# Performance work log

Hardware: AMD Instinct MI355X
Metric: run time of the kernel (lower is better)

The kernel has to match this reference:

```python
import jax, jax.numpy as jnp
import numpy as np

# dims
P = 49      # per-participant input dim
G = 8       # group-only (dyadic/triadic) dim
R = 26      # robot input dim
PH = 20     # participant GRU hidden dim
GF = 16     # group_fc output dim
H = 64      # main RNN hidden dim
T = 512     # seq_len
B = 2048    # batch
D = 2 * P + G + R  # 132 total feature dim, layout [p1|p2|group|robot]


def _gru_cell(x, h, Wih, Whh, bih, bhh):
    # torch.nn.GRUCell math: gates ordered (r, z, n)
    gi = x @ Wih.T + bih          # (B, 3*hid)
    gh = h @ Whh.T + bhh          # (B, 3*hid)
    ir, iz, inn = jnp.split(gi, 3, axis=-1)
    hr, hz, hn = jnp.split(gh, 3, axis=-1)
    r = jax.nn.sigmoid(ir + hr)
    z = jax.nn.sigmoid(iz + hz)
    n = jnp.tanh(inn + r * hn)
    return (1.0 - z) * n + z * h


def setup_inputs() -> dict:
    key = jax.random.key(0)
    ks = jax.random.split(key, 16)

    def u(k, shape, fan):
        b = 1.0 / np.sqrt(fan)
        return jax.random.uniform(k, shape, jnp.float32, -b, b)

    rnn_in = GF + R  # 42: group_fc output concat robot slice
    return {
        "sequence": jax.random.normal(ks[0], (T, B, D), jnp.float32),
        # p1 GRUCell
        "p1_Wih": u(ks[1], (3 * PH, P), PH),
        "p1_Whh": u(ks[2], (3 * PH, PH), PH),
        "p1_bih": u(ks[3], (3 * PH,), PH),
        "p1_bhh": u(ks[4], (3 * PH,), PH),
        # p2 GRUCell
        "p2_Wih": u(ks[5], (3 * PH, P), PH),
        "p2_Whh": u(ks[6], (3 * PH, PH), PH),
        "p2_bih": u(ks[7], (3 * PH,), PH),
        "p2_bhh": u(ks[8], (3 * PH,), PH),
        # group_fc: Linear(2*PH+G -> GF) + ReLU
        "g_W": u(ks[9], (GF, 2 * PH + G), 2 * PH + G),
        "g_b": u(ks[10], (GF,), 2 * PH + G),
        # main GRUCell
        "r_Wih": u(ks[11], (3 * H, rnn_in), H),
        "r_Whh": u(ks[12], (3 * H, H), H),
        "r_bih": u(ks[13], (3 * H,), H),
        "r_bhh": u(ks[14], (3 * H,), H),
    }


def reference(sequence, p1_Wih, p1_Whh, p1_bih, p1_bhh,
              p2_Wih, p2_Whh, p2_bih, p2_bhh,
              g_W, g_b, r_Wih, r_Whh, r_bih, r_bhh):
    batch = sequence.shape[1]

    def step(carry, xt):
        h1, h2, h = carry
        # data_helper slices: [p1 | p2 | group | robot]
        x_p1 = xt[:, :P]
        x_p2 = xt[:, P:2 * P]
        x_g = xt[:, 2 * P:2 * P + G]
        x_r = xt[:, 2 * P + G:]
        h1 = _gru_cell(x_p1, h1, p1_Wih, p1_Whh, p1_bih, p1_bhh)
        h2 = _gru_cell(x_p2, h2, p2_Wih, p2_Whh, p2_bih, p2_bhh)
        g = jax.nn.relu(jnp.concatenate([h1, h2, x_g], axis=1) @ g_W.T + g_b)
        inp = jnp.concatenate([g, x_r], axis=1)  # (B, GF+R)
        h = _gru_cell(inp, h, r_Wih, r_Whh, r_bih, r_bhh)
        return (h1, h2, h), h

    init = (jnp.zeros((batch, PH), jnp.float32),
            jnp.zeros((batch, PH), jnp.float32),
            jnp.zeros((batch, H), jnp.float32))
    _, all_hidden = jax.lax.scan(step, init, sequence)  # (T, B, H)
    return all_hidden
```

## Files before the change

### kernel.cpp

```cpp
#include <hip/hip_runtime.h>


#define T_STEPS 512
#define B_BATCH 2048
#define D_IN    132
#define NROWS   8
#define NBLOCKS 256
#define STEP2   (B_BATCH * D_IN / 2)
#define NITEMS  (NROWS * 66)

typedef _Float16 f16x8 __attribute__((ext_vector_type(8)));
typedef float    f32x4 __attribute__((ext_vector_type(4)));
typedef float    f32x2 __attribute__((ext_vector_type(2)));

#define MFMA16(a, b, c) __builtin_amdgcn_mfma_f32_16x16x32_f16((a), (b), (c), 0, 0, 0)

#define PX    1024
#define AP1   0
#define AP2   2048
#define AG    4096
#define AR    8192
#define AP1H  12288
#define AP2H  14336
#define AH    16384
#define LDS_N 18432

#define BARRIER() do { \
    asm volatile("s_waitcnt lgkmcnt(0)\n\ts_barrier" ::: "memory"); \
    __builtin_amdgcn_sched_barrier(0); \
  } while (0)

__device__ __forceinline__ int swz(int row, int col) {
  return row * 64 + (((col >> 3) ^ (row & 7)) << 3) + (col & 7);
}

__device__ __forceinline__ f16x8 ldsFrag(const _Float16* lds, int base, int lane, int kt) {
  int row = lane & 7;
  int blk = ((kt << 2) + (lane >> 4)) ^ row;
  return *reinterpret_cast<const f16x8*>(lds + base + row * 64 + blk * 8);
}

__device__ __forceinline__ f16x8 mkfrag(const float* W, int row, int K, int kbase, int lane, bool ok) {
  f16x8 f;
  int k0 = kbase + ((lane >> 4) << 3);
#pragma unroll
  for (int j = 0; j < 8; ++j) {
    int k = k0 + j;
    float v = 0.0f;
    if (ok && k < K) v = W[row * K + k];
    f[j] = (_Float16)v;
  }
  return f;
}

__device__ __forceinline__ float rcpf(float x) { return __builtin_amdgcn_rcpf(x); }
__device__ __forceinline__ float ex2(float x)  { return __builtin_amdgcn_exp2f(x); }

__global__ __launch_bounds__(512, 2) void rnn_fused(
    const float* __restrict__ seq,
    const float* __restrict__ p1Wih, const float* __restrict__ p1Whh,
    const float* __restrict__ p1bih, const float* __restrict__ p1bhh,
    const float* __restrict__ p2Wih, const float* __restrict__ p2Whh,
    const float* __restrict__ p2bih, const float* __restrict__ p2bhh,
    const float* __restrict__ gW,    const float* __restrict__ gb,
    const float* __restrict__ rWih,  const float* __restrict__ rWhh,
    const float* __restrict__ rbih,  const float* __restrict__ rbhh,
    float* __restrict__ out)
{
  __shared__ __align__(16) _Float16 lds[LDS_N];
  const int tid  = threadIdx.x;
  const int lane = tid & 63;
  const int wv   = tid >> 6;
  const bool isR = (wv < 4);
  const int b0   = blockIdx.x * NROWS;
  const int ul   = lane & 15;
  const bool lo  = (lane < 32);
  const int grp4 = ((lane >> 4) & 1) * 4;
  const int row0 = grp4 + (lo ? 0 : 2);
  const float C1 = 1.44269504089f;

  for (int i = tid; i < LDS_N; i += 512) lds[i] = (_Float16)0.0f;

  f16x8 fghr[2], fghz[2], fghn[2], fgir[2], fgiz[2], fgin[2];
  float nbr2 = 0, nbz2 = 0, bin2 = 0, bhn2 = 0;
  float hq2[2] = {0, 0};
  int stAddr[3][2]; int ldIdx[3] = {0, 0, 0};
  bool stOK[3] = {false, false, false}, isP[3] = {false, false, false};
  int ahw2[2] = {0, 0};
  float* outp = nullptr;

  f16x8 pgi0[2], pgi1[2], pgi2[2], pgh0, pgh1, pgh2, fgw[2];
  float nbr = 0, nbz = 0, bin = 0, bhn = 0, gbias = 0;
  float h1q2[2] = {0, 0};
  int apB = 0, aphB = 0, up = 0; bool uok = false;
  int agw2[2] = {0, 0}, aphw2[2] = {0, 0}, arw2[2] = {0, 0};

  if (isR) {
    const int uR = wv * 16 + ul;
    fghr[0] = mkfrag(rWhh,       uR, 64,  0, lane, true);
    fghr[1] = mkfrag(rWhh,       uR, 64, 32, lane, true);
    fghz[0] = mkfrag(rWhh,  64 + uR, 64,  0, lane, true);
    fghz[1] = mkfrag(rWhh,  64 + uR, 64, 32, lane, true);
    fghn[0] = mkfrag(rWhh, 128 + uR, 64,  0, lane, true);
    fghn[1] = mkfrag(rWhh, 128 + uR, 64, 32, lane, true);
    fgir[0] = mkfrag(rWih,       uR, 42,  0, lane, true);
    fgir[1] = mkfrag(rWih,       uR, 42, 32, lane, true);
    fgiz[0] = mkfrag(rWih,  64 + uR, 42,  0, lane, true);
    fgiz[1] = mkfrag(rWih,  64 + uR, 42, 32, lane, true);
    fgin[0] = mkfrag(rWih, 128 + uR, 42,  0, lane, true);
    fgin[1] = mkfrag(rWih, 128 + uR, 42, 32, lane, true);
    nbr2 = -C1 * (rbih[uR] + rbhh[uR]);
    nbz2 = -C1 * (rbih[64 + uR] + rbhh[64 + uR]);
    bin2 = rbih[128 + uR]; bhn2 = rbhh[128 + uR];
    ahw2[0] = AH + swz(row0, uR);
    ahw2[1] = AH + swz(row0 + 1, uR);
#pragma unroll
    for (int it = 0; it < 3; ++it) {
      int ii = it * 256 + (wv * 64 + lane);
      stOK[it] = (ii < NITEMS);
      int iic = stOK[it] ? ii : (NITEMS - 1);
      ldIdx[it] = iic;
      int rr = iic / 66, c2 = iic % 66;
      isP[it] = (c2 < 49);
#pragma unroll
      for (int e = 0; e < 2; ++e) {
        int c = c2 * 2 + e;
        int tb, col;
        if (c < 49)       { tb = AP1; col = c; }
        else if (c < 98)  { tb = AP2; col = c - 49; }
        else if (c < 106) { tb = AG;  col = 40 + (c - 98); }
        else              { tb = AR;  col = 16 + (c - 106); }
        stAddr[it][e] = tb + swz(rr, col);
      }
    }
    outp = out + (size_t)(b0 + row0) * 64 + uR;
  } else {
    const int pw  = wv - 4;
    const int gru = pw >> 1;
    const int s   = pw & 1;
    const float* Wih = gru ? p2Wih : p1Wih;
    const float* Whh = gru ? p2Whh : p1Whh;
    const float* bih = gru ? p2bih : p1bih;
    const float* bhh = gru ? p2bhh : p1bhh;
    up  = s * 16 + ul;
    uok = (up < 20);
    pgi0[0] = mkfrag(Wih,      up, 49,  0, lane, uok);
    pgi0[1] = mkfrag(Wih,      up, 49, 32, lane, uok);
    pgh0    = mkfrag(Whh,      up, 20,  0, lane, uok);
    pgi1[0] = mkfrag(Wih, 20 + up, 49,  0, lane, uok);
    pgi1[1] = mkfrag(Wih, 20 + up, 49, 32, lane, uok);
    pgh1    = mkfrag(Whh, 20 + up, 20,  0, lane, uok);
    pgi2[0] = mkfrag(Wih, 40 + up, 49,  0, lane, uok);
    pgi2[1] = mkfrag(Wih, 40 + up, 49, 32, lane, uok);
    pgh2    = mkfrag(Whh, 40 + up, 20,  0, lane, uok);
    fgw[0]  = mkfrag(gW, ul, 48,  0, lane, true);
    fgw[1]  = mkfrag(gW, ul, 48, 32, lane, true);
    gbias = gb[ul];
    if (uok) {
      nbr = -C1 * (bih[up] + bhh[up]);
      nbz = -C1 * (bih[20 + up] + bhh[20 + up]);
      bin = bih[40 + up]; bhn = bhh[40 + up];
    }
    apB  = gru ? AP2  : AP1;
    aphB = gru ? AP2H : AP1H;
    const int gcol = gru ? (20 + up) : up;
#pragma unroll
    for (int j = 0; j < 2; ++j) {
      agw2[j]  = AG + swz(row0 + j, gcol);
      aphw2[j] = aphB + swz(row0 + j, up);
      arw2[j]  = AR + swz(row0 + j, ul);
    }
  }

  __syncthreads();

  f32x2 rs0[3], rs1[3], rs2[3], rs3[3];
  const f32x2* spR = nullptr;
  if (isR) {
    const f32x2* sp = reinterpret_cast<const f32x2*>(seq) + (size_t)b0 * (D_IN / 2);
#pragma unroll
    for (int it = 0; it < 3; ++it) {
      rs0[it] = sp[ldIdx[it]];
      rs1[it] = sp[(size_t)1 * STEP2 + ldIdx[it]];
      rs2[it] = sp[(size_t)2 * STEP2 + ldIdx[it]];
      rs3[it] = sp[(size_t)3 * STEP2 + ldIdx[it]];
    }
#pragma unroll
    for (int it = 0; it < 3; ++it) if (stOK[it]) {
      lds[stAddr[it][0]] = (_Float16)rs0[it][0];
      lds[stAddr[it][1]] = (_Float16)rs0[it][1];
    }
    spR = sp + (size_t)4 * STEP2;
  }
  __syncthreads();

  const f32x4 Z = {0.0f, 0.0f, 0.0f, 0.0f};

  auto rPhase = [&](int offP, int offGR, int slotA, int ahR, int ahW,
                    bool doMain, bool doStage, f32x2 (&rsStage)[3], f32x2 (&rsLoad)[3],
                    bool advance) {
    f16x8 r0, r1, h0, h1f;
    if (doMain) {
      r0  = ldsFrag(lds, AR + slotA, lane, 0);
      r1  = ldsFrag(lds, AR + slotA, lane, 1);
      h0  = ldsFrag(lds, AH + ahR, lane, 0);
      h1f = ldsFrag(lds, AH + ahR, lane, 1);
    }
#pragma unroll
    for (int it = 0; it < 3; ++it) rsLoad[it] = spR[ldIdx[it]];
    if (advance) spR += STEP2;
    if (doStage) {
#pragma unroll
      for (int it = 0; it < 3; ++it) if (stOK[it]) {
        const int off = isP[it] ? offP : offGR;
        lds[off + stAddr[it][0]] = (_Float16)rsStage[it][0];
        lds[off + stAddr[it][1]] = (_Float16)rsStage[it][1];
      }
    }
    if (doMain) {
      f32x4 cR  = MFMA16(h0, fghr[0], Z);
      f32x4 cZ  = MFMA16(h0, fghz[0], Z);
      f32x4 cHN = MFMA16(h0, fghn[0], Z);
      cR  = MFMA16(h1f, fghr[1], cR);
      cZ  = MFMA16(h1f, fghz[1], cZ);
      cHN = MFMA16(h1f, fghn[1], cHN);
      cR  = MFMA16(r0, fgir[0], cR);  cR  = MFMA16(r1, fgir[1], cR);
      cZ  = MFMA16(r0, fgiz[0], cZ);  cZ  = MFMA16(r1, fgiz[1], cZ);
      f32x4 cIN = MFMA16(r0, fgin[0], Z);
      cIN = MFMA16(r1, fgin[1], cIN);
      float xRv[2] = { lo ? cR[0]  : cR[2],  lo ? cR[1]  : cR[3]  };
      float xZv[2] = { lo ? cZ[0]  : cZ[2],  lo ? cZ[1]  : cZ[3]  };
      float xHv[2] = { lo ? cHN[0] : cHN[2], lo ? cHN[1] : cHN[3] };
      float xIv[2] = { lo ? cIN[0] : cIN[2], lo ? cIN[1] : cIN[3] };
#pragma unroll
      for (int j = 0; j < 2; ++j) {
        float r   = rcpf(1.0f + ex2(fmaf(xRv[j], -C1, nbr2)));
        float z   = rcpf(1.0f + ex2(fmaf(xZv[j], -C1, nbz2)));
        float pre = fmaf(r, xHv[j] + bhn2, xIv[j] + bin2);
        float e2  = ex2(pre * (2.0f * C1));
        float n   = 1.0f - 2.0f * rcpf(1.0f + e2);
        float hv  = fmaf(z, hq2[j] - n, n);
        hq2[j] = hv;
        outp[j * 64] = hv;
        lds[ahW + ahw2[j]] = (_Float16)hv;
      }
      outp += (size_t)B_BATCH * 64;
    }
  };

  auto pPhase = [&](int pj, int agWr, int aphWr, int gSlot, bool doComp, bool doGate) {
    f16x8 a0, a1, ah, g0, g1;
    if (doComp) {
      a0 = ldsFrag(lds, apB + pj, lane, 0);
      a1 = ldsFrag(lds, apB + pj, lane, 1);
      ah = ldsFrag(lds, aphB + pj, lane, 0);
    }
    if (doGate) {
      g0 = ldsFrag(lds, AG + gSlot, lane, 0);
      g1 = ldsFrag(lds, AG + gSlot, lane, 1);
    }
    if (doComp) {
      f32x4 aR  = MFMA16(a0, pgi0[0], Z);
      f32x4 aZ  = MFMA16(a0, pgi1[0], Z);
      f32x4 aIN = MFMA16(a0, pgi2[0], Z);
      f32x4 aHN = MFMA16(ah, pgh2, Z);
      aR  = MFMA16(a1, pgi0[1], aR);  aR = MFMA16(ah, pgh0, aR);
      aZ  = MFMA16(a1, pgi1[1], aZ);  aZ = MFMA16(ah, pgh1, aZ);
      aIN = MFMA16(a1, pgi2[1], aIN);
      float xRv[2] = { lo ? aR[0]  : aR[2],  lo ? aR[1]  : aR[3]  };
      float xZv[2] = { lo ? aZ[0]  : aZ[2],  lo ? aZ[1]  : aZ[3]  };
      float xIv[2] = { lo ? aIN[0] : aIN[2], lo ? aIN[1] : aIN[3] };
      float xHv[2] = { lo ? aHN[0] : aHN[2], lo ? aHN[1] : aHN[3] };
#pragma unroll
      for (int j = 0; j < 2; ++j) {
        float r   = rcpf(1.0f + ex2(fmaf(xRv[j], -C1, nbr)));
        float z   = rcpf(1.0f + ex2(fmaf(xZv[j], -C1, nbz)));
        float pre = fmaf(r, xHv[j] + bhn, xIv[j] + bin);
        float e2  = ex2(pre * (2.0f * C1));
        float n   = 1.0f - 2.0f * rcpf(1.0f + e2);
        float hv  = fmaf(z, h1q2[j] - n, n);
        h1q2[j] = hv;
        if (uok) {
          _Float16 hh = (_Float16)hv;
          lds[agWr + agw2[j]]  = hh;
          lds[aphWr + aphw2[j]] = hh;
        }
      }
    }
    if (doGate) {
      f32x4 cG = MFMA16(g0, fgw[0], Z);
      cG = MFMA16(g1, fgw[1], cG);
      float gv0 = lo ? cG[0] : cG[2], gv1 = lo ? cG[1] : cG[3];
      lds[gSlot + arw2[0]] = (_Float16)fmaxf(gv0 + gbias, 0.0f);
      lds[gSlot + arw2[1]] = (_Float16)fmaxf(gv1 + gbias, 0.0f);
    }
  };

  for (int i = 0; i < T_STEPS / 4; ++i) {
    const bool i0 = (i == 0);
    const int f0 = 4 * i;
    if (isR) rPhase(PX, PX, 2 * PX, PX, 0, !i0, true, rs1, rs0, (f0 + 5 < T_STEPS));
    else     pPhase(0, 0, PX, 3 * PX, true, !i0);
    BARRIER();
    if (isR) rPhase(0, 2 * PX, 3 * PX, 0, PX, !i0, true, rs2, rs1, (f0 + 6 < T_STEPS));
    else     pPhase(PX, PX, 0, 0, true, true);
    BARRIER();
    if (isR) rPhase(PX, 3 * PX, 0, PX, 0, true, true, rs3, rs2, (f0 + 7 < T_STEPS));
    else     pPhase(0, 2 * PX, PX, PX, true, true);
    BARRIER();
    if (isR) rPhase(0, 0, PX, 0, PX, true, (i != T_STEPS / 4 - 1), rs0, rs3,
                    (f0 + 8 < T_STEPS));
    else     pPhase(PX, 3 * PX, 0, 2 * PX, true, true);
    BARRIER();
  }
  if (isR) rPhase(0, 0, 2 * PX, PX, 0, true, false, rs0, rs1, false);
  else     pPhase(0, 0, PX, 3 * PX, false, true);
  BARRIER();
  if (isR) rPhase(0, 0, 3 * PX, 0, PX, true, false, rs0, rs1, false);
}

extern "C" void kernel_launch(void* const* d_in, const int* in_sizes, int n_in,
                              void* d_out, int out_size, void* d_ws, size_t ws_size,
                              hipStream_t stream) {
  (void)in_sizes; (void)n_in; (void)d_ws; (void)ws_size; (void)out_size;
  const float* seq   = (const float*)d_in[0];
  const float* p1Wih = (const float*)d_in[1];
  const float* p1Whh = (const float*)d_in[2];
  const float* p1bih = (const float*)d_in[3];
  const float* p1bhh = (const float*)d_in[4];
  const float* p2Wih = (const float*)d_in[5];
  const float* p2Whh = (const float*)d_in[6];
  const float* p2bih = (const float*)d_in[7];
  const float* p2bhh = (const float*)d_in[8];
  const float* gW    = (const float*)d_in[9];
  const float* gb    = (const float*)d_in[10];
  const float* rWih  = (const float*)d_in[11];
  const float* rWhh  = (const float*)d_in[12];
  const float* rbih  = (const float*)d_in[13];
  const float* rbhh  = (const float*)d_in[14];
  float* out = (float*)d_out;
  hipLaunchKernelGGL(rnn_fused, dim3(NBLOCKS), dim3(512), 0, stream,
                     seq, p1Wih, p1Whh, p1bih, p1bhh,
                     p2Wih, p2Whh, p2bih, p2bhh,
                     gW, gb, rWih, rWhh, rbih, rbhh, out);
}
```

Before: 302.8 us.

## Spread input staging across all eight waves and pack fp16 LDS stores

Input prefetch and LDS staging now use all 512 threads instead of only the four main-RNN waves, so each thread handles up to two items instead of three. The participant waves take their share of the global loads and fp16 stores inside their phase. Where the two converted halves are adjacent and aligned in LDS, they are written as one packed 2xfp16 store instead of two scalar stores. This is meant to shorten the critical R-wave phase, which is the slowest between barriers, at the cost of more register pressure and memory traffic in the participant waves.

```diff
diff --git a/kernel.cpp b/kernel.cpp
--- a/kernel.cpp
+++ b/kernel.cpp
@@ -9,9 +9,10 @@
 #define STEP2   (B_BATCH * D_IN / 2)
 #define NITEMS  (NROWS * 66)
 
-typedef _Float16 f16x8 __attribute__((ext_vector_type(8)));
-typedef float    f32x4 __attribute__((ext_vector_type(4)));
-typedef float    f32x2 __attribute__((ext_vector_type(2)));
+typedef _Float16 f16x8  __attribute__((ext_vector_type(8)));
+typedef _Float16 f16x2v __attribute__((ext_vector_type(2)));
+typedef float    f32x4  __attribute__((ext_vector_type(4)));
+typedef float    f32x2  __attribute__((ext_vector_type(2)));
 
 #define MFMA16(a, b, c) __builtin_amdgcn_mfma_f32_16x16x32_f16((a), (b), (c), 0, 0, 0)
 
@@ -81,11 +82,31 @@
 
   for (int i = tid; i < LDS_N; i += 512) lds[i] = (_Float16)0.0f;
 
+  int stA[2][2]; bool isPc[2], pk[2]; int ldI[2];
+  const bool ok1 = (tid < NITEMS - 512);
+#pragma unroll
+  for (int it = 0; it < 2; ++it) {
+    int ii = it * 512 + tid;
+    int iic = (ii < NITEMS) ? ii : (NITEMS - 1);
+    ldI[it] = iic;
+    int rr = iic / 66, c2 = iic % 66;
+    isPc[it] = (c2 < 49);
+#pragma unroll
+    for (int e = 0; e < 2; ++e) {
+      int c = c2 * 2 + e;
+      int tb, col;
+      if (c < 49)       { tb = AP1; col = c; }
+      else if (c < 98)  { tb = AP2; col = c - 49; }
+      else if (c < 106) { tb = AG;  col = 40 + (c - 98); }
+      else              { tb = AR;  col = 16 + (c - 106); }
+      stA[it][e] = tb + swz(rr, col);
+    }
+    pk[it] = (stA[it][1] == stA[it][0] + 1) && ((stA[it][0] & 1) == 0);
+  }
+
   f16x8 fghr[2], fghz[2], fghn[2], fgir[2], fgiz[2], fgin[2];
   float nbr2 = 0, nbz2 = 0, bin2 = 0, bhn2 = 0;
   float hq2[2] = {0, 0};
-  int stAddr[3][2]; int ldIdx[3] = {0, 0, 0};
-  bool stOK[3] = {false, false, false}, isP[3] = {false, false, false};
   int ahw2[2] = {0, 0};
   float* outp = nullptr;
 
@@ -114,25 +135,6 @@
     bin2 = rbih[128 + uR]; bhn2 = rbhh[128 + uR];
     ahw2[0] = AH + swz(row0, uR);
     ahw2[1] = AH + swz(row0 + 1, uR);
-#pragma unroll
-    for (int it = 0; it < 3; ++it) {
-      int ii = it * 256 + (wv * 64 + lane);
-      stOK[it] = (ii < NITEMS);
-      int iic = stOK[it] ? ii : (NITEMS - 1);
-      ldIdx[it] = iic;
-      int rr = iic / 66, c2 = iic % 66;
-      isP[it] = (c2 < 49);
-#pragma unroll
-      for (int e = 0; e < 2; ++e) {
-        int c = c2 * 2 + e;
-        int tb, col;
-        if (c < 49)       { tb = AP1; col = c; }
-        else if (c < 98)  { tb = AP2; col = c - 49; }
-        else if (c < 106) { tb = AG;  col = 40 + (c - 98); }
-        else              { tb = AR;  col = 16 + (c - 106); }
-        stAddr[it][e] = tb + swz(rr, col);
-      }
-    }
     outp = out + (size_t)(b0 + row0) * 64 + uR;
   } else {
     const int pw  = wv - 4;
@@ -174,30 +176,48 @@
 
   __syncthreads();
 
-  f32x2 rs0[3], rs1[3], rs2[3], rs3[3];
-  const f32x2* spR = nullptr;
-  if (isR) {
-    const f32x2* sp = reinterpret_cast<const f32x2*>(seq) + (size_t)b0 * (D_IN / 2);
-#pragma unroll
-    for (int it = 0; it < 3; ++it) {
-      rs0[it] = sp[ldIdx[it]];
-      rs1[it] = sp[(size_t)1 * STEP2 + ldIdx[it]];
-      rs2[it] = sp[(size_t)2 * STEP2 + ldIdx[it]];
-      rs3[it] = sp[(size_t)3 * STEP2 + ldIdx[it]];
-    }
-#pragma unroll
-    for (int it = 0; it < 3; ++it) if (stOK[it]) {
-      lds[stAddr[it][0]] = (_Float16)rs0[it][0];
-      lds[stAddr[it][1]] = (_Float16)rs0[it][1];
-    }
-    spR = sp + (size_t)4 * STEP2;
-  }
+  auto stWrite = [&](int it, int off, const f32x2& v) {
+    if (pk[it]) {
+      f16x2v pv; pv[0] = (_Float16)v[0]; pv[1] = (_Float16)v[1];
+      *reinterpret_cast<f16x2v*>(&lds[off + stA[it][0]]) = pv;
+    } else {
+      lds[off + stA[it][0]] = (_Float16)v[0];
+      lds[off + stA[it][1]] = (_Float16)v[1];
+    }
+  };
+
+  f32x2 rsA[2], rsB[2], rsC[2], rsD[2];
+  const f32x2* sp = reinterpret_cast<const f32x2*>(seq) + (size_t)b0 * (D_IN / 2);
+  rsA[0] = sp[ldI[0]];
+  rsB[0] = sp[(size_t)1 * STEP2 + ldI[0]];
+  rsC[0] = sp[(size_t)2 * STEP2 + ldI[0]];
+  rsD[0] = sp[(size_t)3 * STEP2 + ldI[0]];
+  if (ok1) {
+    rsA[1] = sp[ldI[1]];
+    rsB[1] = sp[(size_t)1 * STEP2 + ldI[1]];
+    rsC[1] = sp[(size_t)2 * STEP2 + ldI[1]];
+    rsD[1] = sp[(size_t)3 * STEP2 + ldI[1]];
+  }
+  stWrite(0, 0, rsA[0]);
+  if (ok1) stWrite(1, 0, rsA[1]);
+  const f32x2* spR = sp + (size_t)4 * STEP2;
   __syncthreads();
 
   const f32x4 Z = {0.0f, 0.0f, 0.0f, 0.0f};
 
+  auto STAGE = [&](int offP, int offGR, f32x2 (&rsStage)[2], f32x2 (&rsLoad)[2],
+                   bool advance, bool doStage) {
+    rsLoad[0] = spR[ldI[0]];
+    if (ok1) rsLoad[1] = spR[ldI[1]];
+    if (advance) spR += STEP2;
+    if (doStage) {
+      stWrite(0, isPc[0] ? offP : offGR, rsStage[0]);
+      if (ok1) stWrite(1, isPc[1] ? offP : offGR, rsStage[1]);
+    }
+  };
+
   auto rPhase = [&](int offP, int offGR, int slotA, int ahR, int ahW,
-                    bool doMain, bool doStage, f32x2 (&rsStage)[3], f32x2 (&rsLoad)[3],
+                    bool doMain, bool doStage, f32x2 (&rsStage)[2], f32x2 (&rsLoad)[2],
                     bool advance) {
     f16x8 r0, r1, h0, h1f;
     if (doMain) {
@@ -206,17 +226,7 @@
       h0  = ldsFrag(lds, AH + ahR, lane, 0);
       h1f = ldsFrag(lds, AH + ahR, lane, 1);
     }
-#pragma unroll
-    for (int it = 0; it < 3; ++it) rsLoad[it] = spR[ldIdx[it]];
-    if (advance) spR += STEP2;
-    if (doStage) {
-#pragma unroll
-      for (int it = 0; it < 3; ++it) if (stOK[it]) {
-        const int off = isP[it] ? offP : offGR;
-        lds[off + stAddr[it][0]] = (_Float16)rsStage[it][0];
-        lds[off + stAddr[it][1]] = (_Float16)rsStage[it][1];
-      }
-    }
+    STAGE(offP, offGR, rsStage, rsLoad, advance, doStage);
     if (doMain) {
       f32x4 cR  = MFMA16(h0, fghr[0], Z);
       f32x4 cZ  = MFMA16(h0, fghz[0], Z);
@@ -248,7 +258,9 @@
     }
   };
 
-  auto pPhase = [&](int pj, int agWr, int aphWr, int gSlot, bool doComp, bool doGate) {
+  auto pPhase = [&](int pj, int agWr, int aphWr, int gSlot, bool doComp, bool doGate,
+                    int offP, int offGR, bool doStage,
+                    f32x2 (&rsStage)[2], f32x2 (&rsLoad)[2], bool advance) {
     f16x8 a0, a1, ah, g0, g1;
     if (doComp) {
       a0 = ldsFrag(lds, apB + pj, lane, 0);
@@ -259,6 +271,7 @@
       g0 = ldsFrag(lds, AG + gSlot, lane, 0);
       g1 = ldsFrag(lds, AG + gSlot, lane, 1);
     }
+    STAGE(offP, offGR, rsStage, rsLoad, advance, doStage);
     if (doComp) {
       f32x4 aR  = MFMA16(a0, pgi0[0], Z);
       f32x4 aZ  = MFMA16(a0, pgi1[0], Z);
@@ -298,25 +311,25 @@
 
   for (int i = 0; i < T_STEPS / 4; ++i) {
     const bool i0 = (i == 0);
+    const bool il = (i == T_STEPS / 4 - 1);
     const int f0 = 4 * i;
-    if (isR) rPhase(PX, PX, 2 * PX, PX, 0, !i0, true, rs1, rs0, (f0 + 5 < T_STEPS));
-    else     pPhase(0, 0, PX, 3 * PX, true, !i0);
+    if (isR) rPhase(PX, PX, 2 * PX, PX, 0, !i0, true, rsB, rsA, (f0 + 5 < T_STEPS));
+    else     pPhase(0, 0, PX, 3 * PX, true, !i0, PX, PX, true, rsB, rsA, (f0 + 5 < T_STEPS));
     BARRIER();
-    if (isR) rPhase(0, 2 * PX, 3 * PX, 0, PX, !i0, true, rs2, rs1, (f0 + 6 < T_STEPS));
-    else     pPhase(PX, PX, 0, 0, true, true);
+    if (isR) rPhase(0, 2 * PX, 3 * PX, 0, PX, !i0, true, rsC, rsB, (f0 + 6 < T_STEPS));
+    else     pPhase(PX, PX, 0, 0, true, true, 0, 2 * PX, true, rsC, rsB, (f0 + 6 < T_STEPS));
     BARRIER();
-    if (isR) rPhase(PX, 3 * PX, 0, PX, 0, true, true, rs3, rs2, (f0 + 7 < T_STEPS));
-    else     pPhase(0, 2 * PX, PX, PX, true, true);
+    if (isR) rPhase(PX, 3 * PX, 0, PX, 0, true, true, rsD, rsC, (f0 + 7 < T_STEPS));
+    else     pPhase(0, 2 * PX, PX, PX, true, true, PX, 3 * PX, true, rsD, rsC, (f0 + 7 < T_STEPS));
     BARRIER();
-    if (isR) rPhase(0, 0, PX, 0, PX, true, (i != T_STEPS / 4 - 1), rs0, rs3,
-                    (f0 + 8 < T_STEPS));
-    else     pPhase(PX, 3 * PX, 0, 2 * PX, true, true);
+    if (isR) rPhase(0, 0, PX, 0, PX, true, !il, rsA, rsD, (f0 + 8 < T_STEPS));
+    else     pPhase(PX, 3 * PX, 0, 2 * PX, true, true, 0, 0, !il, rsA, rsD, (f0 + 8 < T_STEPS));
     BARRIER();
   }
-  if (isR) rPhase(0, 0, 2 * PX, PX, 0, true, false, rs0, rs1, false);
-  else     pPhase(0, 0, PX, 3 * PX, false, true);
+  if (isR) rPhase(0, 0, 2 * PX, PX, 0, true, false, rsA, rsB, false);
+  else     pPhase(0, 0, PX, 3 * PX, false, true, 0, 0, false, rsA, rsB, false);
   BARRIER();
-  if (isR) rPhase(0, 0, 3 * PX, 0, PX, true, false, rs0, rs1, false);
+  if (isR) rPhase(0, 0, 3 * PX, 0, PX, true, false, rsA, rsB, false);
 }
 
 extern "C" void kernel_launch(void* const* d_in, const int* in_sizes, int n_in,
```

Result: slower. 334.7 us (+10.5%).
